# Kernel tuning notes

Hardware: AMD Instinct MI355X
Metric: run time of the kernel (lower is better)

Reference implementation:

```python
import jax, jax.numpy as jnp
import numpy as np


def setup_inputs() -> dict:
    key = jax.random.key(0)
    k1, k2, k3, k4 = jax.random.split(key, 4)
    b, c, h, w = 16, 1024, 32, 32
    dim = h * w  # 1024
    x = jax.random.normal(k1, (b, c, h, w), dtype=jnp.float32)
    cond_img = jax.random.normal(k2, (b, c, h, w), dtype=jnp.float32)
    # torch nn.Linear weights: (out_features, in_features), y = x @ W.T
    Wq = jax.random.normal(k3, (dim, dim), dtype=jnp.float32) * (dim ** -0.5)
    Wkv = jax.random.normal(k4, (2 * dim, dim), dtype=jnp.float32) * (dim ** -0.5)
    return {"x": x, "cond_img": cond_img, "Wq": Wq, "Wkv": Wkv}


def reference(x, cond_img, Wq, Wkv):
    b, c, h, w = x.shape
    dim = h * w
    scale = dim ** -0.5
    xf = x.reshape(b, c, dim)          # (b, c, dim)
    cf = cond_img.reshape(b, c, dim)   # (b, c, dim)
    q = jnp.einsum('bcd,od->bco', xf, Wq)          # (b, c, dim)
    kv = jnp.einsum('bcd,od->bco', cf, Wkv)        # (b, c, 2*dim)
    k, v = jnp.split(kv, 2, axis=-1)               # each (b, c, dim)
    attn = jnp.einsum('bic,bjc->bij', q, k) * scale  # (b, c, c)
    attn = jax.nn.softmax(attn, axis=-1)
    out = jnp.einsum('bij,bjc->bic', attn, v)      # (b, c, dim)
    return out.reshape(b, c, h, w)
```

## Files before the change

### kernel.cpp

```cpp
#include <hip/hip_runtime.h>
#include <stdint.h>


typedef __bf16 bf16_t;
typedef bf16_t bf16x8 __attribute__((ext_vector_type(8)));
typedef float f32x4 __attribute__((ext_vector_type(4)));

#define AS1 __attribute__((address_space(1)))
#define AS3 __attribute__((address_space(3)))

__device__ __forceinline__ uint16_t f2bf(float f) {
  bf16_t h = (bf16_t)f;
  return __builtin_bit_cast(uint16_t, h);
}

__global__ __launch_bounds__(256) void cvt_bf16(const float* __restrict__ in,
                                                uint16_t* __restrict__ out, int n4) {
  int i = blockIdx.x * 256 + threadIdx.x;
  if (i >= n4) return;
  float4 v = ((const float4*)in)[i];
  ushort4 o;
  o.x = f2bf(v.x); o.y = f2bf(v.y); o.z = f2bf(v.z); o.w = f2bf(v.w);
  ((ushort4*)out)[i] = o;
}

__device__ __forceinline__ void stage32(const uint16_t* __restrict__ g, int ldK,
                                        uint16_t* lds, int tid) {
#pragma unroll
  for (int i = 0; i < 2; ++i) {
    int c = i * 512 + tid;
    int row = c >> 2;
    int ch = c & 3;
    int sch = ch ^ ((row >> 1) & 3);
    const uint16_t* gp = g + row * ldK + sch * 8;
    __builtin_amdgcn_global_load_lds((AS1 void*)gp,
                                     (AS3 void*)((uint8_t*)lds + c * 16), 16, 0,
                                     0);
  }
}

template <int MODE>
__global__ __launch_bounds__(512, 2) void gemm_bt(
    const uint16_t* __restrict__ A, const uint16_t* __restrict__ B,
    void* __restrict__ C0, void* __restrict__ C1, int K, int N,
    long long sA, long long sB, long long sC, float scale) {
  __shared__ uint16_t As[4][8192];
  __shared__ uint16_t Bs[4][8192];

  const int tid = threadIdx.x;
  const int lane = tid & 63;
  const int wid = tid >> 6;
  const int wr = wid >> 2;
  const int wc = wid & 3;
  const int lr = lane & 15, lg = lane >> 4;
  const int chnk = ((lg ^ ((lr >> 1) & 3)) << 4);

  const int gx = gridDim.x, gy = gridDim.y;
  const int nwg = gx * gy * gridDim.z;
  int fid = blockIdx.x + gx * (blockIdx.y + gy * blockIdx.z);
  int swz = (fid & 7) * (nwg >> 3) + (fid >> 3);
  const int bx = swz % gx;
  const int rem = swz / gx;
  const int by = rem % gy;
  const int bz = rem / gy;

  const int row0 = by * 256;
  const int col0 = bx * 256;
  const uint16_t* At = A + (long long)bz * sA + (long long)row0 * K;
  const uint16_t* Bt = B + (long long)bz * sB + (long long)col0 * K;

  const int NT = K >> 5;

  stage32(At, K, &As[0][0], tid);
  stage32(Bt, K, &Bs[0][0], tid);
  stage32(At + 32, K, &As[1][0], tid);
  stage32(Bt + 32, K, &Bs[1][0], tid);
  stage32(At + 64, K, &As[2][0], tid);
  stage32(Bt + 64, K, &Bs[2][0], tid);
  asm volatile("s_waitcnt vmcnt(8)" ::: "memory");
  __builtin_amdgcn_s_barrier();

  f32x4 acc[8][4] = {};

  for (int t = 0; t < NT; ++t) {
    const uint16_t* sa = &As[t & 3][0];
    const uint16_t* sb = &Bs[t & 3][0];
    const int tp = t + 3;

    bf16x8 fa[8], fb0, fb1;
#pragma unroll
    for (int mi = 0; mi < 8; ++mi)
      fa[mi] = *(const bf16x8*)((const uint8_t*)sa +
                                (wr * 128 + mi * 16 + lr) * 64 + chnk);
    fb0 = *(const bf16x8*)((const uint8_t*)sb + (wc * 64 + 0 * 16 + lr) * 64 +
                           chnk);
    fb1 = *(const bf16x8*)((const uint8_t*)sb + (wc * 64 + 1 * 16 + lr) * 64 +
                           chnk);
    if (tp < NT) stage32(At + tp * 32, K, &As[tp & 3][0], tid);
    __builtin_amdgcn_s_barrier();
    __builtin_amdgcn_s_setprio(1);
#pragma unroll
    for (int mi = 0; mi < 8; ++mi) {
      acc[mi][0] = __builtin_amdgcn_mfma_f32_16x16x32_bf16(fa[mi], fb0,
                                                           acc[mi][0], 0, 0, 0);
      acc[mi][1] = __builtin_amdgcn_mfma_f32_16x16x32_bf16(fa[mi], fb1,
                                                           acc[mi][1], 0, 0, 0);
    }
    __builtin_amdgcn_s_setprio(0);
    __builtin_amdgcn_s_barrier();

    bf16x8 fb2, fb3;
    fb2 = *(const bf16x8*)((const uint8_t*)sb + (wc * 64 + 2 * 16 + lr) * 64 +
                           chnk);
    fb3 = *(const bf16x8*)((const uint8_t*)sb + (wc * 64 + 3 * 16 + lr) * 64 +
                           chnk);
    if (tp < NT) stage32(Bt + tp * 32, K, &Bs[tp & 3][0], tid);
    __builtin_amdgcn_s_barrier();
    __builtin_amdgcn_s_setprio(1);
#pragma unroll
    for (int mi = 0; mi < 8; ++mi) {
      acc[mi][2] = __builtin_amdgcn_mfma_f32_16x16x32_bf16(fa[mi], fb2,
                                                           acc[mi][2], 0, 0, 0);
      acc[mi][3] = __builtin_amdgcn_mfma_f32_16x16x32_bf16(fa[mi], fb3,
                                                           acc[mi][3], 0, 0, 0);
    }
    __builtin_amdgcn_s_setprio(0);
    if (t + 3 < NT)
      asm volatile("s_waitcnt vmcnt(8)" ::: "memory");
    else if (t + 2 < NT)
      asm volatile("s_waitcnt vmcnt(4)" ::: "memory");
    else if (t + 1 < NT)
      asm volatile("s_waitcnt vmcnt(0)" ::: "memory");
    __builtin_amdgcn_s_barrier();
  }

#pragma unroll
  for (int mi = 0; mi < 8; ++mi) {
#pragma unroll
    for (int ni = 0; ni < 4; ++ni) {
      const int row = row0 + wr * 128 + mi * 16 + lg * 4;
      const int col = col0 + wc * 64 + ni * 16 + lr;
      if (MODE == 0) {
        uint16_t* C = (uint16_t*)C0;
#pragma unroll
        for (int j = 0; j < 4; ++j)
          C[(long long)(row + j) * N + col] = f2bf(acc[mi][ni][j]);
      } else if (MODE == 1) {
        if (col < 1024) {
          uint16_t* Kp = (uint16_t*)C0;
#pragma unroll
          for (int j = 0; j < 4; ++j)
            Kp[(long long)(row + j) * 1024 + col] = f2bf(acc[mi][ni][j]);
        } else {
          const int b = row >> 10, jj = row & 1023;
          ushort4 o;
          o.x = f2bf(acc[mi][ni][0]);
          o.y = f2bf(acc[mi][ni][1]);
          o.z = f2bf(acc[mi][ni][2]);
          o.w = f2bf(acc[mi][ni][3]);
          uint16_t* Vp = (uint16_t*)C1;
          *(ushort4*)(Vp + (long long)b * 1048576 +
                      (long long)(col - 1024) * 1024 + jj) = o;
        }
      } else {
        float* C = (float*)C0;
#pragma unroll
        for (int j = 0; j < 4; ++j)
          C[(long long)bz * sC + (long long)(row + j) * N + col] =
              acc[mi][ni][j] * scale;
      }
    }
  }
}

__global__ __launch_bounds__(256) void softmax_rows(const float* __restrict__ S,
                                                    uint16_t* __restrict__ P) {
  const int row = blockIdx.x;
  const int t = threadIdx.x;
  const int w = t >> 6, l = t & 63;
  __shared__ float red[8];

  const float4 v = ((const float4*)(S + (long long)row * 1024))[t];
  float m = fmaxf(fmaxf(v.x, v.y), fmaxf(v.z, v.w));
#pragma unroll
  for (int o = 1; o < 64; o <<= 1) m = fmaxf(m, __shfl_xor(m, o, 64));
  if (l == 0) red[w] = m;
  __syncthreads();
  m = fmaxf(fmaxf(red[0], red[1]), fmaxf(red[2], red[3]));

  float e0 = __expf(v.x - m), e1 = __expf(v.y - m);
  float e2 = __expf(v.z - m), e3 = __expf(v.w - m);
  float s = e0 + e1 + e2 + e3;
#pragma unroll
  for (int o = 1; o < 64; o <<= 1) s += __shfl_xor(s, o, 64);
  if (l == 0) red[4 + w] = s;
  __syncthreads();
  s = red[4] + red[5] + red[6] + red[7];
  const float inv = 1.0f / s;

  ushort4 o4;
  o4.x = f2bf(e0 * inv); o4.y = f2bf(e1 * inv);
  o4.z = f2bf(e2 * inv); o4.w = f2bf(e3 * inv);
  ((ushort4*)P)[(long long)row * 256 + t] = o4;
}

extern "C" void kernel_launch(void* const* d_in, const int* in_sizes, int n_in,
                              void* d_out, int out_size, void* d_ws, size_t ws_size,
                              hipStream_t stream) {
  const float* x    = (const float*)d_in[0];
  const float* cond = (const float*)d_in[1];
  const float* Wq   = (const float*)d_in[2];
  const float* Wkv  = (const float*)d_in[3];
  float* out = (float*)d_out;

  uint8_t* ws = (uint8_t*)d_ws;
  const long long MiB = 1ll << 20;
  uint16_t* XB   = (uint16_t*)(ws + 0 * MiB);
  uint16_t* CB   = (uint16_t*)(ws + 32 * MiB);
  float*    S    = (float*)(ws + 0 * MiB);
  uint16_t* WQB  = (uint16_t*)(ws + 64 * MiB);
  uint16_t* WKVB = (uint16_t*)(ws + 66 * MiB);
  uint16_t* Q    = (uint16_t*)(ws + 70 * MiB);
  uint16_t* Kb   = (uint16_t*)(ws + 102 * MiB);
  uint16_t* VT   = (uint16_t*)(ws + 134 * MiB);

  cvt_bf16<<<16384, 256, 0, stream>>>(x, XB, 16777216 / 4);
  cvt_bf16<<<16384, 256, 0, stream>>>(cond, CB, 16777216 / 4);
  cvt_bf16<<<1024, 256, 0, stream>>>(Wq, WQB, 1048576 / 4);
  cvt_bf16<<<2048, 256, 0, stream>>>(Wkv, WKVB, 2097152 / 4);

  gemm_bt<0><<<dim3(4, 64, 1), 512, 0, stream>>>(XB, WQB, Q, nullptr, 1024,
                                                 1024, 0, 0, 0, 1.0f);
  gemm_bt<1><<<dim3(8, 64, 1), 512, 0, stream>>>(CB, WKVB, Kb, VT, 1024, 2048,
                                                 0, 0, 0, 1.0f);
  gemm_bt<2><<<dim3(4, 4, 16), 512, 0, stream>>>(Q, Kb, S, nullptr, 1024, 1024,
                                                 1048576, 1048576, 1048576,
                                                 0.03125f);
  softmax_rows<<<16384, 256, 0, stream>>>(S, Q);
  gemm_bt<2><<<dim3(4, 4, 16), 512, 0, stream>>>(Q, VT, out, nullptr, 1024,
                                                 1024, 1048576, 1048576,
                                                 1048576, 1.0f);
}
```

Before: 263.0 us.

## Use BK=64 double-buffered GEMM, LDS-transposed V epilogue, fused conversion kernel

Restructures the GEMM main loop from four 32-wide K stages to two 64-wide stages, with an 8-way XOR swizzle and A fragments for the next tile prefetched between the two MFMA halves. This is meant to halve barriers per K element and overlap LDS reads with compute. The transposed V write in the KV projection now goes through LDS so the global stores are coalesced 16-byte rows. The four fp32-to-bf16 conversion launches are merged into one kernel to cut launch overhead. Shallower buffering may expose more global-load latency.

```diff
diff --git a/kernel.cpp b/kernel.cpp
--- a/kernel.cpp
+++ b/kernel.cpp
@@ -14,28 +14,38 @@
   return __builtin_bit_cast(uint16_t, h);
 }
 
-__global__ __launch_bounds__(256) void cvt_bf16(const float* __restrict__ in,
-                                                uint16_t* __restrict__ out, int n4) {
-  int i = blockIdx.x * 256 + threadIdx.x;
-  if (i >= n4) return;
-  float4 v = ((const float4*)in)[i];
+__global__ __launch_bounds__(256) void cvt_all(
+    const float* __restrict__ x, const float* __restrict__ c,
+    const float* __restrict__ wq, const float* __restrict__ wkv,
+    uint16_t* __restrict__ XB, uint16_t* __restrict__ CB,
+    uint16_t* __restrict__ WQB, uint16_t* __restrict__ WKVB) {
+  long i = (long)blockIdx.x * 256 + threadIdx.x;
+  if (i >= 9175040) return;
+  const float* src;
+  uint16_t* dst;
+  long off;
+  if (i < 4194304) { src = x; dst = XB; off = i; }
+  else if (i < 8388608) { src = c; dst = CB; off = i - 4194304; }
+  else if (i < 8650752) { src = wq; dst = WQB; off = i - 8388608; }
+  else { src = wkv; dst = WKVB; off = i - 8650752; }
+  float4 v = ((const float4*)src)[off];
   ushort4 o;
   o.x = f2bf(v.x); o.y = f2bf(v.y); o.z = f2bf(v.z); o.w = f2bf(v.w);
-  ((ushort4*)out)[i] = o;
-}
-
-__device__ __forceinline__ void stage32(const uint16_t* __restrict__ g, int ldK,
-                                        uint16_t* lds, int tid) {
-#pragma unroll
-  for (int i = 0; i < 2; ++i) {
-    int c = i * 512 + tid;
-    int row = c >> 2;
-    int ch = c & 3;
-    int sch = ch ^ ((row >> 1) & 3);
+  ((ushort4*)dst)[off] = o;
+}
+
+__device__ __forceinline__ void stage_tile(const uint16_t* __restrict__ g,
+                                           int ldK, uint16_t* lds, int tid) {
+#pragma unroll
+  for (int i = 0; i < 4; ++i) {
+    int cix = i * 512 + tid;
+    int row = cix >> 3;
+    int ch = cix & 7;
+    int sch = ch ^ (row & 7);
     const uint16_t* gp = g + row * ldK + sch * 8;
     __builtin_amdgcn_global_load_lds((AS1 void*)gp,
-                                     (AS3 void*)((uint8_t*)lds + c * 16), 16, 0,
-                                     0);
+                                     (AS3 void*)((uint8_t*)lds + cix * 16), 16,
+                                     0, 0);
   }
 }
 
@@ -44,8 +54,7 @@
     const uint16_t* __restrict__ A, const uint16_t* __restrict__ B,
     void* __restrict__ C0, void* __restrict__ C1, int K, int N,
     long long sA, long long sB, long long sC, float scale) {
-  __shared__ uint16_t As[4][8192];
-  __shared__ uint16_t Bs[4][8192];
+  __shared__ uint16_t smem[65536];
 
   const int tid = threadIdx.x;
   const int lane = tid & 63;
@@ -53,7 +62,7 @@
   const int wr = wid >> 2;
   const int wc = wid & 3;
   const int lr = lane & 15, lg = lane >> 4;
-  const int chnk = ((lg ^ ((lr >> 1) & 3)) << 4);
+  const int ch0 = lr & 7;
 
   const int gx = gridDim.x, gy = gridDim.y;
   const int nwg = gx * gy * gridDim.z;
@@ -69,99 +78,134 @@
   const uint16_t* At = A + (long long)bz * sA + (long long)row0 * K;
   const uint16_t* Bt = B + (long long)bz * sB + (long long)col0 * K;
 
-  const int NT = K >> 5;
-
-  stage32(At, K, &As[0][0], tid);
-  stage32(Bt, K, &Bs[0][0], tid);
-  stage32(At + 32, K, &As[1][0], tid);
-  stage32(Bt + 32, K, &Bs[1][0], tid);
-  stage32(At + 64, K, &As[2][0], tid);
-  stage32(Bt + 64, K, &Bs[2][0], tid);
+  const int NT = K >> 6;
+
+  stage_tile(At, K, smem, tid);
+  stage_tile(Bt, K, smem + 32768, tid);
+  stage_tile(At + 64, K, smem + 16384, tid);
+  stage_tile(Bt + 64, K, smem + 49152, tid);
   asm volatile("s_waitcnt vmcnt(8)" ::: "memory");
   __builtin_amdgcn_s_barrier();
 
   f32x4 acc[8][4] = {};
+  bf16x8 aA_[4][2];
+  bf16x8 aB_[4][2];
+  bf16x8 bF[4][2];
+
+  {
+    const uint8_t* sa = (const uint8_t*)smem;
+#pragma unroll
+    for (int mi = 0; mi < 4; ++mi)
+#pragma unroll
+      for (int kk = 0; kk < 2; ++kk)
+        aA_[mi][kk] = *(const bf16x8*)(sa + (wr * 128 + mi * 16 + lr) * 128 +
+                                       (((kk * 4 + lg) ^ ch0) << 4));
+  }
 
   for (int t = 0; t < NT; ++t) {
-    const uint16_t* sa = &As[t & 3][0];
-    const uint16_t* sb = &Bs[t & 3][0];
-    const int tp = t + 3;
-
-    bf16x8 fa[8], fb0, fb1;
-#pragma unroll
-    for (int mi = 0; mi < 8; ++mi)
-      fa[mi] = *(const bf16x8*)((const uint8_t*)sa +
-                                (wr * 128 + mi * 16 + lr) * 64 + chnk);
-    fb0 = *(const bf16x8*)((const uint8_t*)sb + (wc * 64 + 0 * 16 + lr) * 64 +
-                           chnk);
-    fb1 = *(const bf16x8*)((const uint8_t*)sb + (wc * 64 + 1 * 16 + lr) * 64 +
-                           chnk);
-    if (tp < NT) stage32(At + tp * 32, K, &As[tp & 3][0], tid);
+    const uint8_t* sa = (const uint8_t*)(smem + (t & 1) * 16384);
+    const uint8_t* sb = (const uint8_t*)(smem + 32768 + (t & 1) * 16384);
+
+#pragma unroll
+    for (int nj = 0; nj < 4; ++nj)
+#pragma unroll
+      for (int kk = 0; kk < 2; ++kk)
+        bF[nj][kk] =
+            *(const bf16x8*)(sb + (wc * 64 + nj * 16 + lr) * 128 +
+                             (((kk * 4 + lg) ^ ch0) << 4));
+#pragma unroll
+    for (int mi = 0; mi < 4; ++mi)
+#pragma unroll
+      for (int kk = 0; kk < 2; ++kk)
+        aB_[mi][kk] =
+            *(const bf16x8*)(sa + (wr * 128 + 64 + mi * 16 + lr) * 128 +
+                             (((kk * 4 + lg) ^ ch0) << 4));
+    __builtin_amdgcn_s_setprio(1);
+#pragma unroll
+    for (int kk = 0; kk < 2; ++kk)
+#pragma unroll
+      for (int mi = 0; mi < 4; ++mi)
+#pragma unroll
+        for (int nj = 0; nj < 4; ++nj)
+          acc[mi][nj] = __builtin_amdgcn_mfma_f32_16x16x32_bf16(
+              aA_[mi][kk], bF[nj][kk], acc[mi][nj], 0, 0, 0);
+    __builtin_amdgcn_s_setprio(0);
+    if (t + 1 < NT) asm volatile("s_waitcnt vmcnt(4)" ::: "memory");
+    asm volatile("s_waitcnt lgkmcnt(0)" ::: "memory");
     __builtin_amdgcn_s_barrier();
+
+    if (t + 2 < NT) {
+      stage_tile(At + (t + 2) * 64, K, smem + (t & 1) * 16384, tid);
+      stage_tile(Bt + (t + 2) * 64, K, smem + 32768 + (t & 1) * 16384, tid);
+    }
+    if (t + 1 < NT) {
+      const uint8_t* sa2 = (const uint8_t*)(smem + ((t + 1) & 1) * 16384);
+#pragma unroll
+      for (int mi = 0; mi < 4; ++mi)
+#pragma unroll
+        for (int kk = 0; kk < 2; ++kk)
+          aA_[mi][kk] =
+              *(const bf16x8*)(sa2 + (wr * 128 + mi * 16 + lr) * 128 +
+                               (((kk * 4 + lg) ^ ch0) << 4));
+    }
     __builtin_amdgcn_s_setprio(1);
 #pragma unroll
-    for (int mi = 0; mi < 8; ++mi) {
-      acc[mi][0] = __builtin_amdgcn_mfma_f32_16x16x32_bf16(fa[mi], fb0,
-                                                           acc[mi][0], 0, 0, 0);
-      acc[mi][1] = __builtin_amdgcn_mfma_f32_16x16x32_bf16(fa[mi], fb1,
-                                                           acc[mi][1], 0, 0, 0);
-    }
+    for (int kk = 0; kk < 2; ++kk)
+#pragma unroll
+      for (int mi = 0; mi < 4; ++mi)
+#pragma unroll
+        for (int nj = 0; nj < 4; ++nj)
+          acc[4 + mi][nj] = __builtin_amdgcn_mfma_f32_16x16x32_bf16(
+              aB_[mi][kk], bF[nj][kk], acc[4 + mi][nj], 0, 0, 0);
     __builtin_amdgcn_s_setprio(0);
-    __builtin_amdgcn_s_barrier();
-
-    bf16x8 fb2, fb3;
-    fb2 = *(const bf16x8*)((const uint8_t*)sb + (wc * 64 + 2 * 16 + lr) * 64 +
-                           chnk);
-    fb3 = *(const bf16x8*)((const uint8_t*)sb + (wc * 64 + 3 * 16 + lr) * 64 +
-                           chnk);
-    if (tp < NT) stage32(Bt + tp * 32, K, &Bs[tp & 3][0], tid);
-    __builtin_amdgcn_s_barrier();
-    __builtin_amdgcn_s_setprio(1);
-#pragma unroll
-    for (int mi = 0; mi < 8; ++mi) {
-      acc[mi][2] = __builtin_amdgcn_mfma_f32_16x16x32_bf16(fa[mi], fb2,
-                                                           acc[mi][2], 0, 0, 0);
-      acc[mi][3] = __builtin_amdgcn_mfma_f32_16x16x32_bf16(fa[mi], fb3,
-                                                           acc[mi][3], 0, 0, 0);
-    }
-    __builtin_amdgcn_s_setprio(0);
-    if (t + 3 < NT)
+    if (t + 2 < NT)
       asm volatile("s_waitcnt vmcnt(8)" ::: "memory");
-    else if (t + 2 < NT)
-      asm volatile("s_waitcnt vmcnt(4)" ::: "memory");
-    else if (t + 1 < NT)
+    else
       asm volatile("s_waitcnt vmcnt(0)" ::: "memory");
     __builtin_amdgcn_s_barrier();
   }
 
+  if (MODE == 1 && col0 >= 1024) {
+    __syncthreads();
+#pragma unroll
+    for (int mi = 0; mi < 8; ++mi) {
+#pragma unroll
+      for (int ni = 0; ni < 4; ++ni) {
+        const int cc = wc * 64 + ni * 16 + lr;
+        const int jjb = wr * 128 + mi * 16 + lg * 4;
+        ushort4 o;
+        o.x = f2bf(acc[mi][ni][0]);
+        o.y = f2bf(acc[mi][ni][1]);
+        o.z = f2bf(acc[mi][ni][2]);
+        o.w = f2bf(acc[mi][ni][3]);
+        *(ushort4*)&smem[cc * 256 + (jjb ^ ((cc & 7) << 3))] = o;
+      }
+    }
+    __syncthreads();
+    const int b = row0 >> 10, jj0 = row0 & 1023;
+    uint16_t* Vp = (uint16_t*)C1;
+#pragma unroll
+    for (int k = 0; k < 16; ++k) {
+      const int cc = k * 16 + (tid >> 5);
+      const int jb = (tid & 31) * 8;
+      bf16x8 v = *(const bf16x8*)&smem[cc * 256 + (jb ^ ((cc & 7) << 3))];
+      *(bf16x8*)(Vp + (long long)b * 1048576 +
+                 (long long)(col0 - 1024 + cc) * 1024 + jj0 + jb) = v;
+    }
+    return;
+  }
 #pragma unroll
   for (int mi = 0; mi < 8; ++mi) {
 #pragma unroll
     for (int ni = 0; ni < 4; ++ni) {
       const int row = row0 + wr * 128 + mi * 16 + lg * 4;
       const int col = col0 + wc * 64 + ni * 16 + lr;
-      if (MODE == 0) {
+      if (MODE == 0 || MODE == 1) {
         uint16_t* C = (uint16_t*)C0;
 #pragma unroll
         for (int j = 0; j < 4; ++j)
-          C[(long long)(row + j) * N + col] = f2bf(acc[mi][ni][j]);
-      } else if (MODE == 1) {
-        if (col < 1024) {
-          uint16_t* Kp = (uint16_t*)C0;
-#pragma unroll
-          for (int j = 0; j < 4; ++j)
-            Kp[(long long)(row + j) * 1024 + col] = f2bf(acc[mi][ni][j]);
-        } else {
-          const int b = row >> 10, jj = row & 1023;
-          ushort4 o;
-          o.x = f2bf(acc[mi][ni][0]);
-          o.y = f2bf(acc[mi][ni][1]);
-          o.z = f2bf(acc[mi][ni][2]);
-          o.w = f2bf(acc[mi][ni][3]);
-          uint16_t* Vp = (uint16_t*)C1;
-          *(ushort4*)(Vp + (long long)b * 1048576 +
-                      (long long)(col - 1024) * 1024 + jj) = o;
-        }
+          C[(long long)(row + j) * (MODE == 1 ? 1024 : N) + col] =
+              f2bf(acc[mi][ni][j]);
       } else {
         float* C = (float*)C0;
 #pragma unroll
@@ -224,10 +268,7 @@
   uint16_t* Kb   = (uint16_t*)(ws + 102 * MiB);
   uint16_t* VT   = (uint16_t*)(ws + 134 * MiB);
 
-  cvt_bf16<<<16384, 256, 0, stream>>>(x, XB, 16777216 / 4);
-  cvt_bf16<<<16384, 256, 0, stream>>>(cond, CB, 16777216 / 4);
-  cvt_bf16<<<1024, 256, 0, stream>>>(Wq, WQB, 1048576 / 4);
-  cvt_bf16<<<2048, 256, 0, stream>>>(Wkv, WKVB, 2097152 / 4);
+  cvt_all<<<35840, 256, 0, stream>>>(x, cond, Wq, Wkv, XB, CB, WQB, WKVB);
 
   gemm_bt<0><<<dim3(4, 64, 1), 512, 0, stream>>>(XB, WQB, Q, nullptr, 1024,
                                                  1024, 0, 0, 0, 1.0f);
```

New measurement: 239.7 us. 1.1x faster.
